# Optimization experiments

Hardware: AMD Instinct MI355X
Metric: run time of the kernel (lower is better)

The kernel has to match this reference:

```python
import jax, jax.numpy as jnp
import numpy as np

B_, C_, H_, W_, N_ = 2, 256, 64, 64, 16


def setup_inputs() -> dict:
    key = jax.random.key(0)
    ks = jax.random.split(key, 6)
    return {
        "features": jax.random.normal(ks[0], (B_, C_, H_, W_), jnp.float32),
        "A_log": jax.random.normal(ks[1], (C_, N_), jnp.float32) * 0.5,
        "D": jax.random.normal(ks[2], (C_,), jnp.float32),
        "W_delta": jax.random.normal(ks[3], (C_, C_), jnp.float32) * 0.02,
        "b_delta": jnp.zeros((C_,), jnp.float32),
        "W_B": jax.random.normal(ks[4], (C_, N_), jnp.float32) * 0.02,
        "W_C": jax.random.normal(ks[5], (C_, N_), jnp.float32) * 0.02,
    }


def _selective_scan(x, A_log, D, W_delta, b_delta, W_B, W_C):
    # x: (B, L, C) -> (B, L, C). Canonical S6 selective scan (mamba corrector).
    delta = jax.nn.softplus(x @ W_delta + b_delta)          # (B, L, C)
    Bm = x @ W_B                                            # (B, L, N)
    Cm = x @ W_C                                            # (B, L, N)
    A = -jnp.exp(A_log)                                     # (C, N), negative real
    dA = jnp.exp(delta[..., None] * A)                      # (B, L, C, N)
    dBx = (delta * x)[..., None] * Bm[:, :, None, :]        # (B, L, C, N)

    def combine(left, right):
        a_l, b_l = left
        a_r, b_r = right
        return (a_l * a_r, a_r * b_l + b_r)

    # h_t = dA_t * h_{t-1} + dBx_t, computed in parallel over L
    _, h = jax.lax.associative_scan(combine, (dA, dBx), axis=1)
    y = jnp.einsum('blcn,bln->blc', h, Cm) + x * D          # (B, L, C)
    return y


def reference(features, A_log, D, W_delta, b_delta, W_B, W_C):
    B, C, H, W = features.shape
    corr = lambda x: _selective_scan(x, A_log, D, W_delta, b_delta, W_B, W_C)

    # direction 1: row-major forward
    flat = features.reshape(B, C, H * W).transpose(0, 2, 1)        # (B, HW, C)
    out1 = corr(flat)
    # direction 2: row-major reversed
    out2 = jnp.flip(corr(jnp.flip(flat, axis=1)), axis=1)
    # direction 3: rows flipped vertically (flip over H), scan, flip back
    rows = features.transpose(0, 2, 3, 1)                          # (B, H, W, C)
    rows_f = jnp.flip(rows, axis=1).reshape(B, H * W, C)
    out3 = jnp.flip(corr(rows_f).reshape(B, H, W, C), axis=1).reshape(B, H * W, C)
    # direction 4: column-major, flipped over W, scan, flip + transpose back
    cols = features.transpose(0, 3, 2, 1)                          # (B, W, H, C)
    cols_f = jnp.flip(cols, axis=1).reshape(B, W * H, C)
    out4 = jnp.flip(corr(cols_f).reshape(B, W, H, C), axis=1)
    out4 = out4.transpose(0, 2, 1, 3).reshape(B, H * W, C)

    mamba_out = (out1 + out2 + out3 + out4) / 4                    # (B, HW, C)
    return mamba_out.transpose(0, 2, 1).reshape(B, C, H, W)
```

## Files before the change

### kernel.cpp

```cpp
#include <hip/hip_runtime.h>
#include <cstdint>
#include <cstddef>

#define BB 2
#define CC 256
#define NN 16
#define LL 4096
#define NCH 128
#define CLEN 32
#define LCH 8
#define LOG2E 1.4426950408889634f

__device__ __forceinline__ float softplus_f(float z) {
    return fmaxf(z, 0.f) + log1pf(expf(-fabsf(z)));
}

__device__ __forceinline__ uint32_t pack_bf2(float d, float u) {
    uint32_t lo = (__float_as_uint(d) + 0x8000u) >> 16;
    uint32_t hh = (__float_as_uint(u) + 0x8000u) & 0xffff0000u;
    return hh | lo;
}

__global__ __launch_bounds__(256) void k1_delta_gemm(
    const float* __restrict__ feat, const float* __restrict__ Wd,
    const float* __restrict__ bd, const float* __restrict__ WB,
    const float* __restrict__ WC, uint32_t* __restrict__ du,
    float* __restrict__ Bm, float* __restrict__ Cm)
{
    int lc = blockIdx.x & 511;
    int b  = blockIdx.x >> 9;
    int l0 = lc * LCH;
    const float* fbase = feat + (size_t)b * CC * LL;

    int c4   = threadIdx.x & 63;
    int kq   = __builtin_amdgcn_readfirstlane(threadIdx.x >> 6);
    int hi   = (threadIdx.x >> 5) & 1;
    int slot = threadIdx.x & 31;
    int mat  = slot >> 4;
    int n    = slot & 15;
    const float* wBC = mat ? WC : WB;

    float accM[8][4] = {};
    float accB[4] = {};

    int kbase = kq * 64;
    #pragma unroll 4
    for (int kk = 0; kk < 64; ++kk) {
        int k = kbase + kk;
        const float* frow = fbase + (size_t)k * LL + l0;
        float4 x0 = *(const float4*)(frow);
        float4 x1 = *(const float4*)(frow + 4);
        float4 wv = *(const float4*)&Wd[(size_t)k * CC + (c4 << 2)];
        float wb  = wBC[k * NN + n];
        float xs[8] = {x0.x, x0.y, x0.z, x0.w, x1.x, x1.y, x1.z, x1.w};
        #pragma unroll
        for (int l = 0; l < 8; ++l) {
            accM[l][0] = fmaf(xs[l], wv.x, accM[l][0]);
            accM[l][1] = fmaf(xs[l], wv.y, accM[l][1]);
            accM[l][2] = fmaf(xs[l], wv.z, accM[l][2]);
            accM[l][3] = fmaf(xs[l], wv.w, accM[l][3]);
        }
        accB[0] = fmaf(hi ? x0.y : x0.x, wb, accB[0]);
        accB[1] = fmaf(hi ? x0.w : x0.z, wb, accB[1]);
        accB[2] = fmaf(hi ? x1.y : x1.x, wb, accB[2]);
        accB[3] = fmaf(hi ? x1.w : x1.z, wb, accB[3]);
    }

    __shared__ float red[4 * 8 * 64 * 4];
    __shared__ float redBC[4 * 2 * 32 * 4];
    #pragma unroll
    for (int l = 0; l < 8; ++l)
        *(float4*)&red[((kq * 8 + l) * 64 + c4) * 4] =
            make_float4(accM[l][0], accM[l][1], accM[l][2], accM[l][3]);
    *(float4*)&redBC[((kq * 2 + hi) * 32 + slot) * 4] =
        make_float4(accB[0], accB[1], accB[2], accB[3]);
    __syncthreads();

    {
        int lr = threadIdx.x >> 5, slotr = threadIdx.x & 31;
        int jj = lr >> 1, hh = lr & 1;
        float s = 0.f;
        #pragma unroll
        for (int q = 0; q < 4; ++q)
            s += redBC[((q * 2 + hh) * 32 + slotr) * 4 + jj];
        int mr = slotr >> 4, nr = slotr & 15;
        (mr ? Cm : Bm)[((size_t)b * LL + l0 + lr) * NN + nr] = s;
    }

    float4 bd4 = *(const float4*)&bd[c4 << 2];
    float2 vx[4];
    #pragma unroll
    for (int j = 0; j < 4; ++j)
        vx[j] = *(const float2*)&fbase[(size_t)(c4 * 4 + j) * LL + l0 + kq * 2];
    #pragma unroll
    for (int lo = 0; lo < 2; ++lo) {
        int l = kq * 2 + lo;
        float z0 = 0.f, z1 = 0.f, z2 = 0.f, z3 = 0.f;
        #pragma unroll
        for (int q = 0; q < 4; ++q) {
            float4 p = *(float4*)&red[((q * 8 + l) * 64 + c4) * 4];
            z0 += p.x; z1 += p.y; z2 += p.z; z3 += p.w;
        }
        float d0 = softplus_f(z0 + bd4.x);
        float d1 = softplus_f(z1 + bd4.y);
        float d2 = softplus_f(z2 + bd4.z);
        float d3 = softplus_f(z3 + bd4.w);
        float x0v = lo ? vx[0].y : vx[0].x;
        float x1v = lo ? vx[1].y : vx[1].x;
        float x2v = lo ? vx[2].y : vx[2].x;
        float x3v = lo ? vx[3].y : vx[3].x;
        uint4 o;
        o.x = pack_bf2(d0, d0 * x0v);
        o.y = pack_bf2(d1, d1 * x1v);
        o.z = pack_bf2(d2, d2 * x2v);
        o.w = pack_bf2(d3, d3 * x3v);
        *(uint4*)&du[((size_t)b * LL + l0 + l) * CC + (c4 << 2)] = o;
    }
}

__global__ __launch_bounds__(256) void p1_aggr(
    const uint32_t* __restrict__ du, const float* __restrict__ Bm,
    const float* __restrict__ A_log, float* __restrict__ P, float* __restrict__ S)
{
    int blk = blockIdx.x;
    int cls = blk >> 8;
    int b   = (blk >> 7) & 1;
    int ch  = blk & 127;
    int p0, inner;
    if (cls == 0)      { p0 = 32 * ch;        inner = 1; }
    else if (cls == 1) { p0 = 4095 - 32 * ch; inner = -1; }
    else               { p0 = 63 - (ch >> 1) + 2048 * (ch & 1); inner = 64; }
    int c = threadIdx.x;
    __shared__ float sBm[CLEN * NN];
    for (int i = threadIdx.x; i < CLEN * NN; i += 256) {
        int j = i >> 4, nn = i & 15;
        sBm[i] = Bm[((size_t)b * LL + (p0 + inner * j)) * NN + nn];
    }
    const uint32_t* dub = du + (size_t)b * LL * CC + c;
    uint32_t w[CLEN];
    #pragma unroll
    for (int j = 0; j < CLEN; ++j)
        w[j] = dub[(size_t)(p0 + inner * j) * CC];
    float A2[NN];
    {
        const float4* al = (const float4*)(A_log + c * NN);
        #pragma unroll
        for (int q = 0; q < 4; ++q) {
            float4 v = al[q];
            A2[q*4+0] = -expf(v.x) * LOG2E;
            A2[q*4+1] = -expf(v.y) * LOG2E;
            A2[q*4+2] = -expf(v.z) * LOG2E;
            A2[q*4+3] = -expf(v.w) * LOG2E;
        }
    }
    __syncthreads();
    float Sv[NN] = {};
    float sumd = 0.f;
    #pragma unroll
    for (int j = 0; j < CLEN; ++j) {
        float dx = __uint_as_float(w[j] << 16);
        float uy = __uint_as_float(w[j] & 0xffff0000u);
        sumd += dx;
        float dA[NN];
        #pragma unroll
        for (int nn = 0; nn < NN; ++nn) dA[nn] = __builtin_amdgcn_exp2f(A2[nn] * dx);
        #pragma unroll
        for (int nn = 0; nn < NN; ++nn)
            Sv[nn] = fmaf(dA[nn], Sv[nn], uy * sBm[j * 16 + nn]);
    }
    size_t base = ((size_t)((cls * 2 + b) * 128 + ch)) * 4096 + (size_t)c * 16;
    #pragma unroll
    for (int nn = 0; nn < NN; ++nn) {
        P[base + nn] = __builtin_amdgcn_exp2f(A2[nn] * sumd);
        S[base + nn] = Sv[nn];
    }
}

__global__ __launch_bounds__(128) void p2_scan(
    const float* __restrict__ P, const float* __restrict__ S, float* __restrict__ Hin)
{
    int r = blockIdx.x * 128 + threadIdx.x;
    int cn = r & 4095;
    int db = r >> 12;
    int d = db >> 1;
    int cls = (d == 1) ? 1 : ((d == 3) ? 2 : 0);
    int b = db & 1;
    const size_t cbase = ((size_t)(cls * 2 + b) * 128) * 4096 + cn;
    const size_t obase = ((size_t)db * 128) * 4096 + cn;
    float h = 0.f;
    for (int g = 0; g < 16; ++g) {
        float pv[8], sv[8];
        #pragma unroll
        for (int i = 0; i < 8; ++i) {
            int ch = g * 8 + i;
            int chm = (d == 2) ? (126 - 2 * (ch >> 1) + (ch & 1)) : ch;
            size_t ix = cbase + (size_t)chm * 4096;
            pv[i] = P[ix];
            sv[i] = S[ix];
        }
        #pragma unroll
        for (int i = 0; i < 8; ++i) {
            Hin[obase + (size_t)(g * 8 + i) * 4096] = h;
            h = fmaf(pv[i], h, sv[i]);
        }
    }
}

__global__ __launch_bounds__(256) void p3_replay(
    const uint32_t* __restrict__ du, const float* __restrict__ Bm,
    const float* __restrict__ Cm, const float* __restrict__ A_log,
    const float* __restrict__ Hin, float* __restrict__ yA,
    float* __restrict__ yB, float* __restrict__ yC)
{
    int blk = blockIdx.x;
    int sec = blk >> 8;
    int b   = (blk >> 7) & 1;
    int ch  = blk & 127;
    int p0, inner;
    if (sec == 0)      { p0 = 32 * ch;        inner = 1; }
    else if (sec == 1) { p0 = 4095 - 32 * ch; inner = -1; }
    else               { p0 = 63 - (ch >> 1) + 2048 * (ch & 1); inner = 64; }
    int c = threadIdx.x;
    __shared__ float sBm[CLEN * NN];
    __shared__ float sCm[CLEN * NN];
    for (int i = threadIdx.x; i < CLEN * NN; i += 256) {
        int j = i >> 4, nn = i & 15;
        size_t o = ((size_t)b * LL + (p0 + inner * j)) * NN + nn;
        sBm[i] = Bm[o];
        sCm[i] = Cm[o];
    }
    const uint32_t* dub = du + (size_t)b * LL * CC + c;
    uint32_t w[CLEN];
    #pragma unroll
    for (int j = 0; j < CLEN; ++j)
        w[j] = dub[(size_t)(p0 + inner * j) * CC];
    float A2[NN];
    {
        const float4* al = (const float4*)(A_log + c * NN);
        #pragma unroll
        for (int q = 0; q < 4; ++q) {
            float4 v = al[q];
            A2[q*4+0] = -expf(v.x) * LOG2E;
            A2[q*4+1] = -expf(v.y) * LOG2E;
            A2[q*4+2] = -expf(v.z) * LOG2E;
            A2[q*4+3] = -expf(v.w) * LOG2E;
        }
    }

    if (sec == 0) {
        int ch2 = 126 - (ch & ~1) + (ch & 1);
        float h0[NN], h2[NN];
        {
            const float4* hp0 = (const float4*)(Hin + ((size_t)(0 * 2 + b) * 128 + ch)  * 4096 + (size_t)c * 16);
            const float4* hp2 = (const float4*)(Hin + ((size_t)(2 * 2 + b) * 128 + ch2) * 4096 + (size_t)c * 16);
            #pragma unroll
            for (int q = 0; q < 4; ++q) {
                float4 v0 = hp0[q], v2 = hp2[q];
                h0[q*4+0]=v0.x; h0[q*4+1]=v0.y; h0[q*4+2]=v0.z; h0[q*4+3]=v0.w;
                h2[q*4+0]=v2.x; h2[q*4+1]=v2.y; h2[q*4+2]=v2.z; h2[q*4+3]=v2.w;
            }
        }
        __syncthreads();
        #pragma unroll
        for (int j = 0; j < CLEN; ++j) {
            float dx = __uint_as_float(w[j] << 16);
            float uy = __uint_as_float(w[j] & 0xffff0000u);
            float dA[NN];
            #pragma unroll
            for (int nn = 0; nn < NN; ++nn) dA[nn] = __builtin_amdgcn_exp2f(A2[nn] * dx);
            float y0v = 0.f, y2v = 0.f;
            #pragma unroll
            for (int nn = 0; nn < NN; ++nn) {
                float Bu = uy * sBm[j * 16 + nn];
                float cm = sCm[j * 16 + nn];
                h0[nn] = fmaf(dA[nn], h0[nn], Bu);
                h2[nn] = fmaf(dA[nn], h2[nn], Bu);
                y0v = fmaf(h0[nn], cm, y0v);
                y2v = fmaf(h2[nn], cm, y2v);
            }
            yA[((size_t)b * LL + p0 + j) * CC + c] = 0.25f * (y0v + y2v);
        }
    } else {
        int d = (sec == 1) ? 1 : 3;
        float h[NN];
        {
            const float4* hp = (const float4*)(Hin + ((size_t)(d * 2 + b) * 128 + ch) * 4096 + (size_t)c * 16);
            #pragma unroll
            for (int q = 0; q < 4; ++q) {
                float4 v = hp[q];
                h[q*4+0]=v.x; h[q*4+1]=v.y; h[q*4+2]=v.z; h[q*4+3]=v.w;
            }
        }
        __syncthreads();
        float* yD = (sec == 1) ? yB : yC;
        #pragma unroll
        for (int j = 0; j < CLEN; ++j) {
            float dx = __uint_as_float(w[j] << 16);
            float uy = __uint_as_float(w[j] & 0xffff0000u);
            float dA[NN];
            #pragma unroll
            for (int nn = 0; nn < NN; ++nn) dA[nn] = __builtin_amdgcn_exp2f(A2[nn] * dx);
            float yv = 0.f;
            #pragma unroll
            for (int nn = 0; nn < NN; ++nn) {
                float Bu = uy * sBm[j * 16 + nn];
                h[nn] = fmaf(dA[nn], h[nn], Bu);
                yv = fmaf(h[nn], sCm[j * 16 + nn], yv);
            }
            yD[((size_t)b * LL + p0 + inner * j) * CC + c] = 0.25f * yv;
        }
    }
}

__global__ __launch_bounds__(256) void k6_reduce(
    const float* __restrict__ feat, const float* __restrict__ D,
    const float* __restrict__ yA, const float* __restrict__ yB,
    const float* __restrict__ yC, float* __restrict__ out)
{
    int pt = blockIdx.x & 63;
    int ct = (blockIdx.x >> 6) & 3;
    int b  = blockIdx.x >> 8;
    int p0 = pt * 64, c0 = ct * 64;
    __shared__ float tile[64 * 65];
    {
        int cl = threadIdx.x & 63;
        int pg = threadIdx.x >> 6;
        #pragma unroll
        for (int pp = 0; pp < 16; ++pp) {
            int pl = pp * 4 + pg;
            size_t ix = ((size_t)b * LL + p0 + pl) * CC + c0 + cl;
            tile[cl * 65 + pl] = yA[ix] + yB[ix] + yC[ix];
        }
    }
    __syncthreads();
    {
        int pl = threadIdx.x & 63;
        int cg = threadIdx.x >> 6;
        #pragma unroll
        for (int cc = 0; cc < 16; ++cc) {
            int cloc = cc * 4 + cg;
            int c = c0 + cloc;
            size_t o = ((size_t)b * CC + c) * LL + p0 + pl;
            out[o] = tile[cloc * 65 + pl] + feat[o] * D[c];
        }
    }
}

extern "C" void kernel_launch(void* const* d_in, const int* in_sizes, int n_in,
                              void* d_out, int out_size, void* d_ws, size_t ws_size,
                              hipStream_t stream)
{
    const float* feat  = (const float*)d_in[0];
    const float* A_log = (const float*)d_in[1];
    const float* D     = (const float*)d_in[2];
    const float* Wd    = (const float*)d_in[3];
    const float* bd    = (const float*)d_in[4];
    const float* WB    = (const float*)d_in[5];
    const float* WC    = (const float*)d_in[6];
    float* out = (float*)d_out;

    float* ws  = (float*)d_ws;
    uint32_t* du = (uint32_t*)ws;
    float* Bm  = ws  + (size_t)2097152;
    float* Cm  = Bm  + (size_t)131072;
    float* P   = Cm  + (size_t)131072;
    float* S   = P   + (size_t)3145728;
    float* Hin = S   + (size_t)3145728;
    float* yA  = Hin + (size_t)4194304;
    float* yB  = yA  + (size_t)2097152;
    float* yC  = yB  + (size_t)2097152;

    k1_delta_gemm<<<1024, 256, 0, stream>>>(feat, Wd, bd, WB, WC, du, Bm, Cm);
    p1_aggr<<<768, 256, 0, stream>>>(du, Bm, A_log, P, S);
    p2_scan<<<256, 128, 0, stream>>>(P, S, Hin);
    p3_replay<<<768, 256, 0, stream>>>(du, Bm, Cm, A_log, Hin, yA, yB, yC);
    k6_reduce<<<512, 256, 0, stream>>>(feat, D, yA, yB, yC, out);
}
```

Before: 159.9 us.

## Replace FP32 FMA projection GEMM with bf16 MFMA tiles

Rewrites the first kernel, which computes the delta/B/C projections, to use 16x16x32 bf16 MFMA instructions. Each block now covers a 32x64 (L x C) output tile instead of the old k-split FMA loop, so the shared-memory reduction goes away. Inputs and weights are rounded to bf16 on load, which lowers the precision of delta, B and C. The global loads are scalar and strided, which may limit how much the matrix units help.

```diff
diff --git a/kernel.cpp b/kernel.cpp
--- a/kernel.cpp
+++ b/kernel.cpp
@@ -8,8 +8,10 @@
 #define LL 4096
 #define NCH 128
 #define CLEN 32
-#define LCH 8
 #define LOG2E 1.4426950408889634f
+
+typedef __attribute__((ext_vector_type(8))) short short8;
+typedef __attribute__((ext_vector_type(4))) float f32x4;
 
 __device__ __forceinline__ float softplus_f(float z) {
     return fmaxf(z, 0.f) + log1pf(expf(-fabsf(z)));
@@ -21,100 +23,82 @@
     return hh | lo;
 }
 
-__global__ __launch_bounds__(256) void k1_delta_gemm(
+__device__ __forceinline__ short bf16r(float f) {
+    return (short)((__float_as_uint(f) + 0x8000u) >> 16);
+}
+
+__global__ __launch_bounds__(256) void k1_mfma(
     const float* __restrict__ feat, const float* __restrict__ Wd,
     const float* __restrict__ bd, const float* __restrict__ WB,
     const float* __restrict__ WC, uint32_t* __restrict__ du,
     float* __restrict__ Bm, float* __restrict__ Cm)
 {
-    int lc = blockIdx.x & 511;
-    int b  = blockIdx.x >> 9;
-    int l0 = lc * LCH;
+    int blk = blockIdx.x;
+    int b  = blk >> 9;
+    int lt = (blk >> 2) & 127;
+    int ct = blk & 3;
+    int l0 = lt * 32, c0 = ct * 64;
     const float* fbase = feat + (size_t)b * CC * LL;
-
-    int c4   = threadIdx.x & 63;
-    int kq   = __builtin_amdgcn_readfirstlane(threadIdx.x >> 6);
-    int hi   = (threadIdx.x >> 5) & 1;
-    int slot = threadIdx.x & 31;
-    int mat  = slot >> 4;
-    int n    = slot & 15;
-    const float* wBC = mat ? WC : WB;
-
-    float accM[8][4] = {};
-    float accB[4] = {};
-
-    int kbase = kq * 64;
-    #pragma unroll 4
-    for (int kk = 0; kk < 64; ++kk) {
-        int k = kbase + kk;
-        const float* frow = fbase + (size_t)k * LL + l0;
-        float4 x0 = *(const float4*)(frow);
-        float4 x1 = *(const float4*)(frow + 4);
-        float4 wv = *(const float4*)&Wd[(size_t)k * CC + (c4 << 2)];
-        float wb  = wBC[k * NN + n];
-        float xs[8] = {x0.x, x0.y, x0.z, x0.w, x1.x, x1.y, x1.z, x1.w};
-        #pragma unroll
-        for (int l = 0; l < 8; ++l) {
-            accM[l][0] = fmaf(xs[l], wv.x, accM[l][0]);
-            accM[l][1] = fmaf(xs[l], wv.y, accM[l][1]);
-            accM[l][2] = fmaf(xs[l], wv.z, accM[l][2]);
-            accM[l][3] = fmaf(xs[l], wv.w, accM[l][3]);
-        }
-        accB[0] = fmaf(hi ? x0.y : x0.x, wb, accB[0]);
-        accB[1] = fmaf(hi ? x0.w : x0.z, wb, accB[1]);
-        accB[2] = fmaf(hi ? x1.y : x1.x, wb, accB[2]);
-        accB[3] = fmaf(hi ? x1.w : x1.z, wb, accB[3]);
-    }
-
-    __shared__ float red[4 * 8 * 64 * 4];
-    __shared__ float redBC[4 * 2 * 32 * 4];
-    #pragma unroll
-    for (int l = 0; l < 8; ++l)
-        *(float4*)&red[((kq * 8 + l) * 64 + c4) * 4] =
-            make_float4(accM[l][0], accM[l][1], accM[l][2], accM[l][3]);
-    *(float4*)&redBC[((kq * 2 + hi) * 32 + slot) * 4] =
-        make_float4(accB[0], accB[1], accB[2], accB[3]);
-    __syncthreads();
-
-    {
-        int lr = threadIdx.x >> 5, slotr = threadIdx.x & 31;
-        int jj = lr >> 1, hh = lr & 1;
-        float s = 0.f;
-        #pragma unroll
-        for (int q = 0; q < 4; ++q)
-            s += redBC[((q * 2 + hh) * 32 + slotr) * 4 + jj];
-        int mr = slotr >> 4, nr = slotr & 15;
-        (mr ? Cm : Bm)[((size_t)b * LL + l0 + lr) * NN + nr] = s;
-    }
-
-    float4 bd4 = *(const float4*)&bd[c4 << 2];
-    float2 vx[4];
-    #pragma unroll
-    for (int j = 0; j < 4; ++j)
-        vx[j] = *(const float2*)&fbase[(size_t)(c4 * 4 + j) * LL + l0 + kq * 2];
-    #pragma unroll
-    for (int lo = 0; lo < 2; ++lo) {
-        int l = kq * 2 + lo;
-        float z0 = 0.f, z1 = 0.f, z2 = 0.f, z3 = 0.f;
-        #pragma unroll
-        for (int q = 0; q < 4; ++q) {
-            float4 p = *(float4*)&red[((q * 8 + l) * 64 + c4) * 4];
-            z0 += p.x; z1 += p.y; z2 += p.z; z3 += p.w;
-        }
-        float d0 = softplus_f(z0 + bd4.x);
-        float d1 = softplus_f(z1 + bd4.y);
-        float d2 = softplus_f(z2 + bd4.z);
-        float d3 = softplus_f(z3 + bd4.w);
-        float x0v = lo ? vx[0].y : vx[0].x;
-        float x1v = lo ? vx[1].y : vx[1].x;
-        float x2v = lo ? vx[2].y : vx[2].x;
-        float x3v = lo ? vx[3].y : vx[3].x;
-        uint4 o;
-        o.x = pack_bf2(d0, d0 * x0v);
-        o.y = pack_bf2(d1, d1 * x1v);
-        o.z = pack_bf2(d2, d2 * x2v);
-        o.w = pack_bf2(d3, d3 * x3v);
-        *(uint4*)&du[((size_t)b * LL + l0 + l) * CC + (c4 << 2)] = o;
+    int lane = threadIdx.x & 63;
+    int wq   = threadIdx.x >> 6;
+    int m    = lane & 15;
+    int quad = lane >> 4;
+    int m0   = (wq & 1) * 16;
+    int n0   = (wq >> 1) * 32;
+    bool doBC = (ct == 0);
+    const float* wBC = (wq >> 1) ? WC : WB;
+
+    f32x4 acc0 = {0.f, 0.f, 0.f, 0.f};
+    f32x4 acc1 = {0.f, 0.f, 0.f, 0.f};
+    f32x4 accB = {0.f, 0.f, 0.f, 0.f};
+
+    const float* aptr  = fbase + (size_t)(quad * 8) * LL + (l0 + m0 + m);
+    const float* b0ptr = Wd    + (size_t)(quad * 8) * CC + (c0 + n0 + m);
+    const float* b1ptr = b0ptr + 16;
+    const float* bbptr = wBC   + (size_t)(quad * 8) * NN + m;
+
+    for (int ks = 0; ks < 8; ++ks) {
+        short8 af, bf0, bf1;
+        #pragma unroll
+        for (int j = 0; j < 8; ++j) {
+            size_t kr = (size_t)(ks * 32 + j);
+            af[j]  = bf16r(aptr [kr * LL]);
+            bf0[j] = bf16r(b0ptr[kr * CC]);
+            bf1[j] = bf16r(b1ptr[kr * CC]);
+        }
+        acc0 = __builtin_amdgcn_mfma_f32_16x16x32_bf16(af, bf0, acc0, 0, 0, 0);
+        acc1 = __builtin_amdgcn_mfma_f32_16x16x32_bf16(af, bf1, acc1, 0, 0, 0);
+        if (doBC) {
+            short8 bbf;
+            #pragma unroll
+            for (int j = 0; j < 8; ++j)
+                bbf[j] = bf16r(bbptr[(size_t)(ks * 32 + j) * NN]);
+            accB = __builtin_amdgcn_mfma_f32_16x16x32_bf16(af, bbf, accB, 0, 0, 0);
+        }
+    }
+
+    if (doBC) {
+        float* dst = (wq >> 1) ? Cm : Bm;
+        #pragma unroll
+        for (int r = 0; r < 4; ++r) {
+            int l = l0 + m0 + quad * 4 + r;
+            dst[((size_t)b * LL + l) * NN + m] = accB[r];
+        }
+    }
+
+    float bd0 = bd[c0 + n0 + m];
+    float bd1 = bd[c0 + n0 + 16 + m];
+    int cA = c0 + n0 + m;
+    int cB = cA + 16;
+    #pragma unroll
+    for (int r = 0; r < 4; ++r) {
+        int l = l0 + m0 + quad * 4 + r;
+        float d0 = softplus_f(acc0[r] + bd0);
+        float d1 = softplus_f(acc1[r] + bd1);
+        float x0 = fbase[(size_t)cA * LL + l];
+        float x1 = fbase[(size_t)cB * LL + l];
+        du[((size_t)b * LL + l) * CC + cA] = pack_bf2(d0, d0 * x0);
+        du[((size_t)b * LL + l) * CC + cB] = pack_bf2(d1, d1 * x1);
     }
 }
 
@@ -370,7 +354,7 @@
     float* yB  = yA  + (size_t)2097152;
     float* yC  = yB  + (size_t)2097152;
 
-    k1_delta_gemm<<<1024, 256, 0, stream>>>(feat, Wd, bd, WB, WC, du, Bm, Cm);
+    k1_mfma<<<1024, 256, 0, stream>>>(feat, Wd, bd, WB, WC, du, Bm, Cm);
     p1_aggr<<<768, 256, 0, stream>>>(du, Bm, A_log, P, S);
     p2_scan<<<256, 128, 0, stream>>>(P, S, Hin);
     p3_replay<<<768, 256, 0, stream>>>(du, Bm, Cm, A_log, Hin, yA, yB, yC);
```

New measurement: 150.0 us. -6.2%, faster.
